# Kernel optimization log

Measured on AMD Instinct MI355X. Metric: run time of the kernel, lower is better.

Reference implementation:

```python
import jax, jax.numpy as jnp
import numpy as np

B, N, D, H = 1024, 32, 512, 4
HD = D // H


def setup_inputs() -> dict:
    key = jax.random.key(0)
    k1, k2, k3 = jax.random.split(key, 3)
    scale = 1.0 / np.sqrt(D)  # keep logits in a sane range (mimics xavier init)
    return {
        "agent_hiddens": jax.random.normal(k1, (B, N, D), dtype=jnp.float32),
        "padding_mask": jnp.zeros((B, N), dtype=bool),
        "in_proj_weight": jax.random.normal(k2, (3 * D, D), dtype=jnp.float32) * scale,
        "in_proj_bias": jnp.zeros((3 * D,), dtype=jnp.float32),
        "out_proj_weight": jax.random.normal(k3, (D, D), dtype=jnp.float32) * scale,
        "out_proj_bias": jnp.zeros((D,), dtype=jnp.float32),
    }


def reference(agent_hiddens, padding_mask, in_proj_weight, in_proj_bias,
              out_proj_weight, out_proj_bias):
    # Equivalent to the per-agent loop: full self-attention over the N agents
    # with the diagonal (self) and padded agents masked out of the keys.
    qkv = agent_hiddens @ in_proj_weight.T + in_proj_bias      # (B, N, 3D)
    q, k, v = jnp.split(qkv, 3, axis=-1)
    # (B, H, N, HD)
    q = q.reshape(B, N, H, HD).transpose(0, 2, 1, 3)
    k = k.reshape(B, N, H, HD).transpose(0, 2, 1, 3)
    v = v.reshape(B, N, H, HD).transpose(0, 2, 1, 3)

    scores = jnp.einsum('bhqd,bhkd->bhqk', q, k) / jnp.sqrt(jnp.float32(HD))
    self_mask = jnp.eye(N, dtype=bool)                         # exclude j == i
    mask = self_mask[None, None, :, :] | padding_mask[:, None, None, :]
    scores = jnp.where(mask, -jnp.inf, scores)
    attn = jax.nn.softmax(scores, axis=-1)                     # (B, H, N, N)

    ctx = jnp.einsum('bhqk,bhkd->bhqd', attn, v)               # (B, H, N, HD)
    ctx = ctx.transpose(0, 2, 1, 3).reshape(B, N, D)
    return ctx @ out_proj_weight.T + out_proj_bias
```

## Files before the change

### kernel.cpp

```cpp
#include <hip/hip_runtime.h>
#include <hip/hip_bf16.h>


typedef __attribute__((ext_vector_type(4))) float  f32x4;
typedef __attribute__((ext_vector_type(8))) short  bf16x8;
typedef __attribute__((ext_vector_type(4))) short  bf16x4;
typedef __attribute__((ext_vector_type(4))) int    i32x4;

__device__ __forceinline__ unsigned short f2bf(float f) {
    unsigned u = __builtin_bit_cast(unsigned, f);
    u = (u + 0x7FFFu + ((u >> 16) & 1u)) >> 16;
    return (unsigned short)u;
}
__device__ __forceinline__ float bf2f(unsigned short h) {
    unsigned u = ((unsigned)h) << 16;
    return __builtin_bit_cast(float, u);
}

__device__ __forceinline__ void gload_lds16(const void* g, void* l) {
    __builtin_amdgcn_global_load_lds(
        (const __attribute__((address_space(1))) void*)g,
        (__attribute__((address_space(3))) void*)l, 16, 0, 0);
}

__global__ __launch_bounds__(256)
void cvt_kernel(const float* __restrict__ src, unsigned short* __restrict__ dst, int n4)
{
    int i = blockIdx.x * 256 + threadIdx.x;
    if (i >= n4) return;
    f32x4 v = ((const f32x4*)src)[i];
    bf16x4 o;
#pragma unroll
    for (int e = 0; e < 4; ++e) o[e] = (short)f2bf(v[e]);
    ((bf16x4*)dst)[i] = o;
}

template<int MODE>
__global__ __launch_bounds__(256)
void gemm_bt(const unsigned short* __restrict__ A, const unsigned short* __restrict__ Bw,
             const float* __restrict__ bias, void* __restrict__ Cout, int ldc, int ntx)
{
    __shared__ unsigned short As[128 * 64];
    __shared__ unsigned short Bs[128 * 64];

    const int t = threadIdx.x;
    const int nwg = gridDim.x;
    const int cpx = nwg >> 3;
    const int lin = blockIdx.x;
    const int swz = (lin & 7) * cpx + (lin >> 3);
    const int bx = swz % ntx, by = swz / ntx;
    const int mbase = by * 128, nbase = bx * 128;

    const int w = t >> 6, l = t & 63;
    const int wr = w >> 1, wc = w & 1;
    const int lg = l >> 4, lr = l & 15;

    f32x4 acc[4][4] = {};

    for (int ks = 0; ks < 512; ks += 64) {
        __syncthreads();
#pragma unroll
        for (int i = 0; i < 4; ++i) {
            int c   = i * 256 + t;
            int row = c >> 3;
            int ke  = (c & 7) * 8;
            gload_lds16(A  + (size_t)(mbase + row) * 512 + ks + ke,
                        &As[(size_t)(i * 256 + w * 64) * 8]);
            gload_lds16(Bw + (size_t)(nbase + row) * 512 + ks + ke,
                        &Bs[(size_t)(i * 256 + w * 64) * 8]);
        }
        __syncthreads();
#pragma unroll
        for (int kk = 0; kk < 64; kk += 32) {
            bf16x8 af[4], bfr[4];
#pragma unroll
            for (int mi = 0; mi < 4; ++mi)
                af[mi] = *(const bf16x8*)&As[(wr * 64 + mi * 16 + lr) * 64 + kk + lg * 8];
#pragma unroll
            for (int ni = 0; ni < 4; ++ni)
                bfr[ni] = *(const bf16x8*)&Bs[(wc * 64 + ni * 16 + lr) * 64 + kk + lg * 8];
#pragma unroll
            for (int mi = 0; mi < 4; ++mi)
#pragma unroll
                for (int ni = 0; ni < 4; ++ni)
                    acc[mi][ni] = __builtin_amdgcn_mfma_f32_16x16x32_bf16(
                        af[mi], bfr[ni], acc[mi][ni], 0, 0, 0);
        }
    }

#pragma unroll
    for (int ni = 0; ni < 4; ++ni) {
        int col = nbase + wc * 64 + ni * 16 + lr;
        float bv = bias[col];
#pragma unroll
        for (int mi = 0; mi < 4; ++mi) {
            int row0 = mbase + wr * 64 + mi * 16 + lg * 4;
#pragma unroll
            for (int ri = 0; ri < 4; ++ri) {
                float v = acc[mi][ni][ri] + bv;
                if (MODE == 0)
                    ((unsigned short*)Cout)[(size_t)(row0 + ri) * ldc + col] = f2bf(v);
                else
                    ((float*)Cout)[(size_t)(row0 + ri) * ldc + col] = v;
            }
        }
    }
}

__global__ __launch_bounds__(256)
void attn_kernel(const unsigned short* __restrict__ qkv,
                 const unsigned char* __restrict__ pad,
                 unsigned short* __restrict__ ctx)
{
    __shared__ f32x4 Qs[32 * 32];
    __shared__ f32x4 Ks[32 * 32];
    __shared__ f32x4 Vs[32 * 32];
    __shared__ float Ps[32 * 33];

    const int bid = blockIdx.x;
    const int b = bid >> 2, h = bid & 3;
    const int t = threadIdx.x;
    const int r = t >> 3, j = t & 7;

    const unsigned short* base = qkv + ((size_t)(b * 32 + r) * 1536 + h * 128);
#pragma unroll
    for (int sel = 0; sel < 3; ++sel) {
        f32x4* dst = (sel == 0) ? Qs : (sel == 1) ? Ks : Vs;
        const unsigned short* src = base + sel * 512 + j * 16;
#pragma unroll
        for (int it = 0; it < 2; ++it) {
            i32x4 raw = *(const i32x4*)(src + it * 8);
            float fv[8];
#pragma unroll
            for (int e = 0; e < 8; ++e) {
                unsigned word = ((const unsigned*)&raw)[e >> 1];
                unsigned short hb = (e & 1) ? (unsigned short)(word >> 16)
                                            : (unsigned short)(word & 0xffffu);
                fv[e] = bf2f(hb);
            }
            int c0 = j * 4 + it * 2;
            f32x4 v0 = {fv[0], fv[1], fv[2], fv[3]};
            f32x4 v1 = {fv[4], fv[5], fv[6], fv[7]};
            dst[r * 32 + ((c0    ) ^ r)] = v0;
            dst[r * 32 + ((c0 + 1) ^ r)] = v1;
        }
    }
    __syncthreads();

    const int q  = r;
    const int kc = j * 4;
    float s[4] = {0.f, 0.f, 0.f, 0.f};
#pragma unroll 4
    for (int d4 = 0; d4 < 32; ++d4) {
        f32x4 qv = Qs[q * 32 + (d4 ^ q)];
#pragma unroll
        for (int jj = 0; jj < 4; ++jj) {
            f32x4 kv = Ks[(kc + jj) * 32 + (d4 ^ (kc + jj))];
#pragma unroll
            for (int e = 0; e < 4; ++e) s[jj] = fmaf(qv[e], kv[e], s[jj]);
        }
    }
    const float sc = 0.08838834764831845f;
    float m = -INFINITY;
#pragma unroll
    for (int jj = 0; jj < 4; ++jj) {
        int kcol = kc + jj;
        bool msk = (kcol == q) || (pad[b * 32 + kcol] != 0);
        s[jj] = msk ? -INFINITY : s[jj] * sc;
        m = fmaxf(m, s[jj]);
    }
    m = fmaxf(m, __shfl_xor(m, 1));
    m = fmaxf(m, __shfl_xor(m, 2));
    m = fmaxf(m, __shfl_xor(m, 4));
    float p[4], sum = 0.f;
#pragma unroll
    for (int jj = 0; jj < 4; ++jj) { p[jj] = __expf(s[jj] - m); sum += p[jj]; }
    sum += __shfl_xor(sum, 1);
    sum += __shfl_xor(sum, 2);
    sum += __shfl_xor(sum, 4);
#pragma unroll
    for (int jj = 0; jj < 4; ++jj) Ps[q * 33 + kc + jj] = p[jj];
    __syncthreads();

    float c[16] = {0.f};
#pragma unroll 4
    for (int k = 0; k < 32; ++k) {
        float pv = Ps[q * 33 + k];
#pragma unroll
        for (int cc = 0; cc < 4; ++cc) {
            f32x4 vv = Vs[k * 32 + ((j + 8 * cc) ^ k)];
#pragma unroll
            for (int e = 0; e < 4; ++e) c[cc * 4 + e] = fmaf(pv, vv[e], c[cc * 4 + e]);
        }
    }
    const float inv = 1.0f / sum;
    unsigned short* co = ctx + (size_t)(b * 32 + q) * 512 + h * 128;
#pragma unroll
    for (int cc = 0; cc < 4; ++cc) {
        bf16x4 ov;
#pragma unroll
        for (int e = 0; e < 4; ++e) ov[e] = (short)f2bf(c[cc * 4 + e] * inv);
        *(bf16x4*)(co + (j + 8 * cc) * 4) = ov;
    }
}

extern "C" void kernel_launch(void* const* d_in, const int* in_sizes, int n_in,
                              void* d_out, int out_size, void* d_ws, size_t ws_size,
                              hipStream_t stream)
{
    const float*         X    = (const float*)d_in[0];
    const unsigned char* pad  = (const unsigned char*)d_in[1];
    const float*         Win  = (const float*)d_in[2];
    const float*         bin  = (const float*)d_in[3];
    const float*         Wout = (const float*)d_in[4];
    const float*         bout = (const float*)d_in[5];
    float*               out  = (float*)d_out;

    char* ws = (char*)d_ws;
    unsigned short* qkvb  = (unsigned short*)(ws);
    unsigned short* Xb    = (unsigned short*)(ws + (size_t)100663296);
    unsigned short* ctxb  = Xb;
    unsigned short* Winb  = (unsigned short*)(ws + (size_t)134217728);
    unsigned short* Woutb = (unsigned short*)(ws + (size_t)135790592);

    dim3 blk(256);
    cvt_kernel<<<dim3(16384), blk, 0, stream>>>(X,    Xb,    4194304);
    cvt_kernel<<<dim3(768),   blk, 0, stream>>>(Win,  Winb,  196608);
    cvt_kernel<<<dim3(256),   blk, 0, stream>>>(Wout, Woutb, 65536);
    gemm_bt<0><<<dim3(3072), blk, 0, stream>>>(Xb, Winb, bin, qkvb, 1536, 12);
    attn_kernel<<<dim3(4096), blk, 0, stream>>>(qkvb, pad, ctxb);
    gemm_bt<1><<<dim3(1024), blk, 0, stream>>>(ctxb, Woutb, bout, out, 512, 4);
}
```

Measured before the change: 313.5 us.

## Double-buffer GEMM LDS tiles with XOR swizzle and fuse the conversion launches

The GEMM now keeps two LDS buffers and issues the global-to-LDS loads for the next k-tile while MFMAs run on the current one, with one barrier per iteration instead of two. Staged tiles use an XOR swizzle on 16-byte chunks so the fragment reads avoid LDS bank conflicts. The three fp32-to-bf16 conversion launches are merged into one kernel to cut launch overhead. LDS use doubles to 64KB per block, which may lower occupancy.

```diff
diff --git a/kernel.cpp b/kernel.cpp
--- a/kernel.cpp
+++ b/kernel.cpp
@@ -24,15 +24,21 @@
 }
 
 __global__ __launch_bounds__(256)
-void cvt_kernel(const float* __restrict__ src, unsigned short* __restrict__ dst, int n4)
+void cvt3_kernel(const float* __restrict__ s0, unsigned short* __restrict__ d0, int n0,
+                 const float* __restrict__ s1, unsigned short* __restrict__ d1, int n1,
+                 const float* __restrict__ s2, unsigned short* __restrict__ d2, int n2)
 {
     int i = blockIdx.x * 256 + threadIdx.x;
-    if (i >= n4) return;
-    f32x4 v = ((const f32x4*)src)[i];
+    const float* s; unsigned short* d; int k;
+    if (i < n0)                { s = s0; d = d0; k = i; }
+    else if (i < n0 + n1)      { s = s1; d = d1; k = i - n0; }
+    else if (i < n0 + n1 + n2) { s = s2; d = d2; k = i - n0 - n1; }
+    else return;
+    f32x4 v = ((const f32x4*)s)[k];
     bf16x4 o;
 #pragma unroll
     for (int e = 0; e < 4; ++e) o[e] = (short)f2bf(v[e]);
-    ((bf16x4*)dst)[i] = o;
+    ((bf16x4*)d)[k] = o;
 }
 
 template<int MODE>
@@ -40,8 +46,8 @@
 void gemm_bt(const unsigned short* __restrict__ A, const unsigned short* __restrict__ Bw,
              const float* __restrict__ bias, void* __restrict__ Cout, int ldc, int ntx)
 {
-    __shared__ unsigned short As[128 * 64];
-    __shared__ unsigned short Bs[128 * 64];
+    __shared__ unsigned short As[2][128 * 64];
+    __shared__ unsigned short Bs[2][128 * 64];
 
     const int t = threadIdx.x;
     const int nwg = gridDim.x;
@@ -55,30 +61,41 @@
     const int wr = w >> 1, wc = w & 1;
     const int lg = l >> 4, lr = l & 15;
 
+    int soff[4];
+#pragma unroll
+    for (int i = 0; i < 4; ++i) {
+        int p = i * 256 + t;
+        int row = p >> 3, pc = p & 7;
+        int lc = pc ^ (row & 7);
+        soff[i] = row * 512 + lc * 8;
+    }
+    const unsigned short* Ab = A  + (size_t)mbase * 512;
+    const unsigned short* Bb = Bw + (size_t)nbase * 512;
+
     f32x4 acc[4][4] = {};
 
-    for (int ks = 0; ks < 512; ks += 64) {
-        __syncthreads();
+    auto STAGE = [&](int buf, int ks) {
 #pragma unroll
         for (int i = 0; i < 4; ++i) {
-            int c   = i * 256 + t;
-            int row = c >> 3;
-            int ke  = (c & 7) * 8;
-            gload_lds16(A  + (size_t)(mbase + row) * 512 + ks + ke,
-                        &As[(size_t)(i * 256 + w * 64) * 8]);
-            gload_lds16(Bw + (size_t)(nbase + row) * 512 + ks + ke,
-                        &Bs[(size_t)(i * 256 + w * 64) * 8]);
-        }
-        __syncthreads();
+            gload_lds16(Ab + soff[i] + ks, &As[buf][(i * 256 + w * 64) * 8]);
+            gload_lds16(Bb + soff[i] + ks, &Bs[buf][(i * 256 + w * 64) * 8]);
+        }
+    };
+    auto COMPUTE = [&](int buf) {
 #pragma unroll
         for (int kk = 0; kk < 64; kk += 32) {
+            const int lc = (kk >> 3) + lg;
             bf16x8 af[4], bfr[4];
 #pragma unroll
-            for (int mi = 0; mi < 4; ++mi)
-                af[mi] = *(const bf16x8*)&As[(wr * 64 + mi * 16 + lr) * 64 + kk + lg * 8];
-#pragma unroll
-            for (int ni = 0; ni < 4; ++ni)
-                bfr[ni] = *(const bf16x8*)&Bs[(wc * 64 + ni * 16 + lr) * 64 + kk + lg * 8];
+            for (int mi = 0; mi < 4; ++mi) {
+                int r = wr * 64 + mi * 16 + lr;
+                af[mi] = *(const bf16x8*)&As[buf][r * 64 + ((lc ^ (r & 7)) << 3)];
+            }
+#pragma unroll
+            for (int ni = 0; ni < 4; ++ni) {
+                int n = wc * 64 + ni * 16 + lr;
+                bfr[ni] = *(const bf16x8*)&Bs[buf][n * 64 + ((lc ^ (n & 7)) << 3)];
+            }
 #pragma unroll
             for (int mi = 0; mi < 4; ++mi)
 #pragma unroll
@@ -86,7 +103,19 @@
                     acc[mi][ni] = __builtin_amdgcn_mfma_f32_16x16x32_bf16(
                         af[mi], bfr[ni], acc[mi][ni], 0, 0, 0);
         }
-    }
+    };
+
+    int cur = 0;
+    STAGE(0, 0);
+    __syncthreads();
+#pragma unroll 1
+    for (int ti = 0; ti < 7; ++ti) {
+        STAGE(cur ^ 1, (ti + 1) << 6);
+        COMPUTE(cur);
+        __syncthreads();
+        cur ^= 1;
+    }
+    COMPUTE(cur);
 
 #pragma unroll
     for (int ni = 0; ni < 4; ++ni) {
@@ -224,9 +253,9 @@
     unsigned short* Woutb = (unsigned short*)(ws + (size_t)135790592);
 
     dim3 blk(256);
-    cvt_kernel<<<dim3(16384), blk, 0, stream>>>(X,    Xb,    4194304);
-    cvt_kernel<<<dim3(768),   blk, 0, stream>>>(Win,  Winb,  196608);
-    cvt_kernel<<<dim3(256),   blk, 0, stream>>>(Wout, Woutb, 65536);
+    cvt3_kernel<<<dim3(17408), blk, 0, stream>>>(X, Xb, 4194304,
+                                                 Win, Winb, 196608,
+                                                 Wout, Woutb, 65536);
     gemm_bt<0><<<dim3(3072), blk, 0, stream>>>(Xb, Winb, bin, qkvb, 1536, 12);
     attn_kernel<<<dim3(4096), blk, 0, stream>>>(qkvb, pad, ctxb);
     gemm_bt<1><<<dim3(1024), blk, 0, stream>>>(ctxb, Woutb, bout, out, 512, 4);
```

After: 289.0 us. 7.8% less time.
